# Optimization experiments

Measured on AMD Instinct MI355X. Metric: run time of the kernel, lower is better.

## Reference

```python
import jax, jax.numpy as jnp
import numpy as np

B, T, H, I, O = 64, 1024, 512, 64, 8
NOISE_STD = 0.05
ALPHA = 0.2


def setup_inputs() -> dict:
    key = jax.random.key(0)
    ks = jax.random.split(key, 5)
    return {
        "input": jax.random.normal(ks[0], (B, T, I), dtype=jnp.float32),
        "noise": jax.random.normal(ks[1], (B, T, H), dtype=jnp.float32),
        "wi": jax.random.normal(ks[2], (I, H), dtype=jnp.float32) / np.float32(np.sqrt(H)),
        "si": jnp.ones((I,), jnp.float32),
        # scale so the all-positive effective recurrence |wrec| stays stable over T steps
        "wrec": jax.random.normal(ks[3], (H, H), dtype=jnp.float32) * np.float32(0.5 / H),
        "b": jnp.zeros((H,), jnp.float32),
        "wo": jax.random.normal(ks[4], (H, O), dtype=jnp.float32) / np.float32(H),
        "so": jnp.ones((O,), jnp.float32),
        "wi_mask": jnp.ones((I, H), jnp.float32),
        "wrec_mask": jnp.ones((H, H), jnp.float32),
        "wo_mask": jnp.ones((H, O), jnp.float32),
        "h0": jnp.zeros((H,), jnp.float32),
    }


def reference(input, noise, wi, si, wrec, b, wo, so, wi_mask, wrec_mask, wo_mask, h0):
    batch = input.shape[0]
    # effective weights (constant across timesteps; torch recomputes identical values each step)
    wrec_eff = jnp.abs(wrec) * wrec_mask            # [H, H]
    wi_eff = (wi * si[:, None]) * wi_mask           # [I, H]
    wo_eff = (wo * so[None, :]) * wo_mask           # [H, O]

    h_init = jnp.broadcast_to(h0, (batch, h0.shape[0]))  # [B, H]

    def step(h, xs):
        x_t, n_t = xs                                # [B, I], [B, H]
        r = jax.nn.relu(h)                           # rate from previous state
        h_new = h + NOISE_STD * n_t + ALPHA * (-h + r @ wrec_eff + b + x_t @ wi_eff)
        out_t = jax.nn.relu(h_new) @ wo_eff          # [B, O]
        return h_new, (out_t, h_new)

    xs = (jnp.swapaxes(input, 0, 1), jnp.swapaxes(noise, 0, 1))  # time-major
    _, (outs, hs) = jax.lax.scan(step, h_init, xs)
    output = jnp.swapaxes(outs, 0, 1)                            # [B, T, O]
    trajectories = jnp.concatenate(
        [h_init[:, None, :], jnp.swapaxes(hs, 0, 1)], axis=1     # [B, T+1, H]
    )
    return output, trajectories
```

## Files before the change

### kernel.cpp

```cpp
#include <hip/hip_runtime.h>
#include <hip/hip_bf16.h>
#include <cstddef>
#include <cstdint>

#define BB 64
#define TT 1024
#define HH 512
#define II 64
#define OO 8
#define NOISE_STD 0.05f
#define ALPHA 0.2f

#define G_SLICES 16
#define BT 4
#define NC (BB/BT)
#define K4EXT 160
#define R2STRIDE 328

typedef _Float16 half2_t __attribute__((ext_vector_type(2)));
typedef unsigned int uint32;
typedef uint32 uint4_t __attribute__((ext_vector_type(4)));

#if __has_builtin(__builtin_amdgcn_fdot2)
__device__ __forceinline__ float fdot2f(half2_t a, half2_t b, float c) {
    return __builtin_amdgcn_fdot2(a, b, c, false);
}
#else
__device__ __forceinline__ float fdot2f(half2_t a, half2_t b, float c) {
    return c + (float)a[0] * (float)b[0] + (float)a[1] * (float)b[1];
}
#endif

__device__ __forceinline__ half2_t pkrtz(float a, float b) {
    return __builtin_bit_cast(half2_t, __builtin_amdgcn_cvt_pkrtz(a, b));
}

__device__ __forceinline__ uint4_t load4_sc1(const uint32* p) {
    uint4_t v;
    asm volatile("global_load_dwordx4 %0, %1, off sc1\n\t"
                 "s_waitcnt vmcnt(0)"
                 : "=v"(v) : "v"(p) : "memory");
    return v;
}
__device__ __forceinline__ uint4_t load4_sc0(const uint32* p) {
    uint4_t v;
    asm volatile("global_load_dwordx4 %0, %1, off sc0\n\t"
                 "s_waitcnt vmcnt(0)"
                 : "=v"(v) : "v"(p) : "memory");
    return v;
}
__device__ __forceinline__ void store1_plain(uint32* p, uint32 v) {
    asm volatile("global_store_dword %0, %1, off" :: "v"(p), "v"(v) : "memory");
}

__global__ __launch_bounds__(512, 2)
void rnn_clique(const float* __restrict__ input, const float* __restrict__ noise,
                const float* __restrict__ wi, const float* __restrict__ si,
                const float* __restrict__ wrec, const float* __restrict__ bvec,
                const float* __restrict__ wo, const float* __restrict__ so,
                const float* __restrict__ wi_mask, const float* __restrict__ wrec_mask,
                const float* __restrict__ wo_mask, const float* __restrict__ h0,
                uint32* __restrict__ ex, float* __restrict__ out,
                float* __restrict__ traj)
{
    const int tid  = threadIdx.x;
    const int cq   = blockIdx.x & 15;
    const int sl   = blockIdx.x >> 4;
    const int wv   = tid >> 6;
    const int lane = tid & 63;

    __shared__ half2_t w2[K4EXT * 64];
    __shared__ half2_t r2[2][BT][R2STRIDE];
    __shared__ float   part[BT][8][32];
    __shared__ half2_t wo2[256];
    __shared__ int     mode_sh;

    uint32* aux = ex + (size_t)NC * 2 * BT * HH;

    if (tid == 0) {
        uint32 xcc;
        asm volatile("s_getreg_b32 %0, hwreg(HW_REG_XCC_ID)" : "=s"(xcc));
        xcc &= 0xFFu;
        __hip_atomic_store(aux + cq * 16 + sl, (1u << 16) | xcc,
                           __ATOMIC_RELAXED, __HIP_MEMORY_SCOPE_AGENT);
    }

    {
        const int c = tid & 31, kg = tid >> 5;
        const int gc = sl * 32 + c;
        for (int m = 0; m < 10; ++m) {
            int k4 = m * 16 + kg;
            float v[4];
            #pragma unroll
            for (int q = 0; q < 4; ++q) {
                int kap = k4 * 4 + q;
                float x;
                if (kap < HH) {
                    x = fabsf(wrec[(size_t)kap * HH + gc]) * wrec_mask[(size_t)kap * HH + gc];
                } else if (kap < HH + II) {
                    int i = kap - HH;
                    x = wi[(size_t)i * HH + gc] * si[i] * wi_mask[(size_t)i * HH + gc];
                } else if (kap == HH + II) {
                    x = bvec[gc];
                } else {
                    x = 0.f;
                }
                v[q] = x;
            }
            w2[k4 * 64 + c * 2]     = pkrtz(v[0], v[1]);
            w2[k4 * 64 + c * 2 + 1] = pkrtz(v[2], v[3]);
        }
    }
    if (sl < OO && tid < 256) {
        int k2 = tid, o = sl;
        float v0 = wo[(size_t)(2 * k2) * OO + o] * so[o] * wo_mask[(size_t)(2 * k2) * OO + o];
        float v1 = wo[(size_t)(2 * k2 + 1) * OO + o] * so[o] * wo_mask[(size_t)(2 * k2 + 1) * OO + o];
        wo2[k2] = pkrtz(v0, v1);
    }
    if (tid < 128) {
        int k4 = tid;
        float v0 = fmaxf(h0[4 * k4 + 0], 0.f), v1 = fmaxf(h0[4 * k4 + 1], 0.f);
        float v2 = fmaxf(h0[4 * k4 + 2], 0.f), v3 = fmaxf(h0[4 * k4 + 3], 0.f);
        half2_t p0 = pkrtz(v0, v1), p1 = pkrtz(v2, v3);
        for (int b = 0; b < BT; ++b) { r2[0][b][2 * k4] = p0; r2[0][b][2 * k4 + 1] = p1; }
    }
    if (tid < 8) {
        int par = tid & 1, b = tid >> 1;
        r2[par][b][288] = half2_t{(_Float16)1.f, (_Float16)0.f};
        for (int s = 289; s < R2STRIDE; ++s) r2[par][b][s] = half2_t{(_Float16)0.f, (_Float16)0.f};
    }
    if (wv >= 4 && lane < 32) {
        int b = wv - 4, i2 = lane;
        const float* xp = input + ((size_t)(cq * BT + b) * TT + 0) * II + 2 * i2;
        r2[0][b][256 + i2] = pkrtz(xp[0], xp[1]);
    }

    float h_st = 0.f, n_reg = 0.f, n_reg2 = 0.f;
    float* trajp = nullptr;
    const float* noisep = nullptr;
    uint32* exw = nullptr;
    if (wv < BT && lane < 32) {
        int b = wv, c = lane, gc = sl * 32 + c, bg = cq * BT + b;
        h_st   = h0[gc];
        noisep = noise + (size_t)bg * TT * HH;
        trajp  = traj + (size_t)bg * (TT + 1) * HH;
        n_reg  = noisep[gc];
        n_reg2 = noisep[(size_t)HH + gc];
        trajp[gc] = h_st;
        exw = ex + (size_t)((cq * 2 + 0) * BT + b) * HH + gc;
    }
    __syncthreads();

    const int c_    = lane & 31;
    const int shalf = lane >> 5;
    const int seg   = wv * 2 + shalf;

    half2_t wr[5][4];
    #pragma unroll
    for (int ch = 0; ch < 5; ++ch) {
        int k4b = seg * 10 + ch * 2;
        wr[ch][0] = w2[k4b * 64 + c_ * 2];
        wr[ch][1] = w2[k4b * 64 + c_ * 2 + 1];
        wr[ch][2] = w2[(k4b + 1) * 64 + c_ * 2];
        wr[ch][3] = w2[(k4b + 1) * 64 + c_ * 2 + 1];
    }

    if (wv == 0) {
        uint32 v = (1u << 16);
        for (;;) {
            if (lane < 16)
                v = __hip_atomic_load(aux + cq * 16 + lane,
                                      __ATOMIC_RELAXED, __HIP_MEMORY_SCOPE_AGENT);
            if (__ballot((v >> 16) == 1u) == ~0ull) break;
            __builtin_amdgcn_s_sleep(1);
        }
        uint32 myx = v & 0xFFFFu;
        uint32 x0  = __shfl(myx, 0);
        bool eq = (lane < 16) ? (myx == x0) : true;
        if (lane == 0) mode_sh = (__ballot(eq) == ~0ull) ? 1 : 0;
    }
    __syncthreads();
    const bool local_mode = (mode_sh != 0);

    const int gb  = tid >> 7;
    const int k4g = tid & 127;
    uint32* exg0 = ex + (size_t)((cq * 2 + 0) * BT + gb) * HH + (size_t)(4 * k4g);
    const size_t expar = (size_t)BT * HH;

    for (int t = 0; t < TT; ++t) {
        const int p = t & 1;

        float acc0 = 0.f, acc1 = 0.f, acc2 = 0.f, acc3 = 0.f;
        #pragma unroll
        for (int ch = 0; ch < 5; ++ch) {
            int k2b = seg * 20 + ch * 4;
            {
                half2_t ra = r2[p][0][k2b], rb = r2[p][0][k2b + 1], rc = r2[p][0][k2b + 2], rd = r2[p][0][k2b + 3];
                acc0 = fdot2f(ra, wr[ch][0], acc0); acc0 = fdot2f(rb, wr[ch][1], acc0);
                acc0 = fdot2f(rc, wr[ch][2], acc0); acc0 = fdot2f(rd, wr[ch][3], acc0);
            }
            {
                half2_t ra = r2[p][1][k2b], rb = r2[p][1][k2b + 1], rc = r2[p][1][k2b + 2], rd = r2[p][1][k2b + 3];
                acc1 = fdot2f(ra, wr[ch][0], acc1); acc1 = fdot2f(rb, wr[ch][1], acc1);
                acc1 = fdot2f(rc, wr[ch][2], acc1); acc1 = fdot2f(rd, wr[ch][3], acc1);
            }
            {
                half2_t ra = r2[p][2][k2b], rb = r2[p][2][k2b + 1], rc = r2[p][2][k2b + 2], rd = r2[p][2][k2b + 3];
                acc2 = fdot2f(ra, wr[ch][0], acc2); acc2 = fdot2f(rb, wr[ch][1], acc2);
                acc2 = fdot2f(rc, wr[ch][2], acc2); acc2 = fdot2f(rd, wr[ch][3], acc2);
            }
            {
                half2_t ra = r2[p][3][k2b], rb = r2[p][3][k2b + 1], rc = r2[p][3][k2b + 2], rd = r2[p][3][k2b + 3];
                acc3 = fdot2f(ra, wr[ch][0], acc3); acc3 = fdot2f(rb, wr[ch][1], acc3);
                acc3 = fdot2f(rc, wr[ch][2], acc3); acc3 = fdot2f(rd, wr[ch][3], acc3);
            }
        }
        acc0 += __shfl_xor(acc0, 32);
        acc1 += __shfl_xor(acc1, 32);
        acc2 += __shfl_xor(acc2, 32);
        acc3 += __shfl_xor(acc3, 32);
        if (shalf == 0) {
            part[0][wv][c_] = acc0;
            part[1][wv][c_] = acc1;
            part[2][wv][c_] = acc2;
            part[3][wv][c_] = acc3;
        }
        __syncthreads();

        const uint32 tag = (uint32)(t + 2);
        const size_t poff = (size_t)p * expar;

        if (wv < BT && lane < 32) {
            int b = wv, c = lane, gc = sl * 32 + c;
            float mv = 0.f;
            #pragma unroll
            for (int m = 0; m < 8; ++m) mv += part[b][m][c];
            float hn = (1.f - ALPHA) * h_st + ALPHA * mv + NOISE_STD * n_reg;
            h_st = hn;
            uint32 r16 = __builtin_bit_cast(uint32,
                           __builtin_amdgcn_cvt_pkrtz(fmaxf(hn, 0.f), 0.f)) & 0xFFFFu;
            uint32 word = (tag << 16) | r16;
            if (local_mode) {
                store1_plain(exw + poff, word);
            } else {
                __hip_atomic_store(exw + poff, word,
                                   __ATOMIC_RELAXED, __HIP_MEMORY_SCOPE_AGENT);
            }
            trajp[(size_t)(t + 1) * HH + gc] = hn;
            n_reg = n_reg2;
            int tn = (t + 2 < TT) ? (t + 2) : (TT - 1);
            n_reg2 = noisep[(size_t)tn * HH + gc];
        } else if (wv >= 4) {
            if (sl < OO && t > 0) {
                int b = wv - 4;
                int k2 = lane * 4;
                float q = 0.f;
                q = fdot2f(r2[p][b][k2],     wo2[k2],     q);
                q = fdot2f(r2[p][b][k2 + 1], wo2[k2 + 1], q);
                q = fdot2f(r2[p][b][k2 + 2], wo2[k2 + 2], q);
                q = fdot2f(r2[p][b][k2 + 3], wo2[k2 + 3], q);
                #pragma unroll
                for (int d = 32; d >= 1; d >>= 1) q += __shfl_xor(q, d);
                if (lane == 0) out[((size_t)(cq * BT + b) * TT + (t - 1)) * OO + sl] = q;
            }
            if (lane < 32) {
                int b = wv - 4, i2 = lane;
                int tn = (t + 1 < TT) ? (t + 1) : (TT - 1);
                const float* xp = input + ((size_t)(cq * BT + b) * TT + tn) * II + 2 * i2;
                r2[p ^ 1][b][256 + i2] = pkrtz(xp[0], xp[1]);
            }
        }

        {
            const uint32* g0 = exg0 + poff;
            uint4_t w;
            int spins = 0;
            if (local_mode) {
                for (;;) {
                    w = load4_sc0(g0);
                    if ((w[0] >> 16) == tag && (w[1] >> 16) == tag &&
                        (w[2] >> 16) == tag && (w[3] >> 16) == tag) break;
                    if (++spins > 8) __builtin_amdgcn_s_sleep(1);
                }
            } else {
                for (;;) {
                    w = load4_sc1(g0);
                    if ((w[0] >> 16) == tag && (w[1] >> 16) == tag &&
                        (w[2] >> 16) == tag && (w[3] >> 16) == tag) break;
                    __builtin_amdgcn_s_sleep(1);
                }
            }
            uint32 q0 = (w[0] & 0xFFFFu) | (w[1] << 16);
            uint32 q1 = (w[2] & 0xFFFFu) | (w[3] << 16);
            r2[p ^ 1][gb][2 * k4g]     = __builtin_bit_cast(half2_t, q0);
            r2[p ^ 1][gb][2 * k4g + 1] = __builtin_bit_cast(half2_t, q1);
        }
        __syncthreads();
    }

    if (wv >= 4 && sl < OO) {
        int b = wv - 4;
        int k2 = lane * 4;
        float q = 0.f;
        q = fdot2f(r2[0][b][k2],     wo2[k2],     q);
        q = fdot2f(r2[0][b][k2 + 1], wo2[k2 + 1], q);
        q = fdot2f(r2[0][b][k2 + 2], wo2[k2 + 2], q);
        q = fdot2f(r2[0][b][k2 + 3], wo2[k2 + 3], q);
        #pragma unroll
        for (int d = 32; d >= 1; d >>= 1) q += __shfl_xor(q, d);
        if (lane == 0) out[((size_t)(cq * BT + b) * TT + (TT - 1)) * OO + sl] = q;
    }
}

extern "C" void kernel_launch(void* const* d_in, const int* in_sizes, int n_in,
                              void* d_out, int out_size, void* d_ws, size_t ws_size,
                              hipStream_t stream) {
    const float* input     = (const float*)d_in[0];
    const float* noise     = (const float*)d_in[1];
    const float* wi        = (const float*)d_in[2];
    const float* si        = (const float*)d_in[3];
    const float* wrec      = (const float*)d_in[4];
    const float* bvec      = (const float*)d_in[5];
    const float* wo        = (const float*)d_in[6];
    const float* so        = (const float*)d_in[7];
    const float* wi_mask   = (const float*)d_in[8];
    const float* wrec_mask = (const float*)d_in[9];
    const float* wo_mask   = (const float*)d_in[10];
    const float* h0        = (const float*)d_in[11];

    float* out  = (float*)d_out;
    float* traj = out + (size_t)BB * TT * OO;
    uint32* ex  = (uint32*)d_ws;

    (void)hipMemsetAsync(d_ws, 0,
        (size_t)(NC * 2 * BT * HH + NC * G_SLICES) * sizeof(uint32), stream);

    rnn_clique<<<dim3(NC * G_SLICES), dim3(512), 0, stream>>>(
        input, noise, wi, si, wrec, bvec, wo, so,
        wi_mask, wrec_mask, wo_mask, h0, ex, out, traj);
}
```

Before: 1.608 ms.

## Interleave two batch groups per block to hide cross-block exchange latency

Each block now handles two groups of four batch rows (A and B) instead of one, which halves the grid to 128 blocks. The time loop alternates between the two groups: the matvec for one group runs while the other group's exchanged hidden state is still in flight through global memory. The aim is to hide the spin-wait latency of the cross-block sync behind useful compute. In exchange each block does twice the work per step with extra __syncthreads, fewer CUs are used, and more LDS is needed for the doubled r2 buffers. The local-mode spin threshold also goes from 8 to 16.

Measured after the change: 3.017 ms. 87.6% more time.

```diff
diff --git a/kernel.cpp b/kernel.cpp
--- a/kernel.cpp
+++ b/kernel.cpp
@@ -11,11 +11,14 @@
 #define NOISE_STD 0.05f
 #define ALPHA 0.2f
 
-#define G_SLICES 16
+#define NCL 8
+#define SLICES 16
 #define BT 4
-#define NC (BB/BT)
 #define K4EXT 160
 #define R2STRIDE 328
+
+#define EXGRP (2 * BT * HH)
+#define EXCQ  (2 * EXGRP)
 
 typedef _Float16 half2_t __attribute__((ext_vector_type(2)));
 typedef unsigned int uint32;
@@ -64,24 +67,24 @@
                 float* __restrict__ traj)
 {
     const int tid  = threadIdx.x;
-    const int cq   = blockIdx.x & 15;
-    const int sl   = blockIdx.x >> 4;
+    const int cq   = blockIdx.x & 7;
+    const int sl   = blockIdx.x >> 3;
     const int wv   = tid >> 6;
     const int lane = tid & 63;
 
     __shared__ half2_t w2[K4EXT * 64];
-    __shared__ half2_t r2[2][BT][R2STRIDE];
+    __shared__ half2_t r2[2][2][BT][R2STRIDE];
     __shared__ float   part[BT][8][32];
     __shared__ half2_t wo2[256];
     __shared__ int     mode_sh;
 
-    uint32* aux = ex + (size_t)NC * 2 * BT * HH;
+    uint32* aux = ex + (size_t)NCL * EXCQ;
 
     if (tid == 0) {
         uint32 xcc;
         asm volatile("s_getreg_b32 %0, hwreg(HW_REG_XCC_ID)" : "=s"(xcc));
         xcc &= 0xFFu;
-        __hip_atomic_store(aux + cq * 16 + sl, (1u << 16) | xcc,
+        __hip_atomic_store(aux + cq * SLICES + sl, (1u << 16) | xcc,
                            __ATOMIC_RELAXED, __HIP_MEMORY_SCOPE_AGENT);
     }
 
@@ -122,32 +125,41 @@
         float v0 = fmaxf(h0[4 * k4 + 0], 0.f), v1 = fmaxf(h0[4 * k4 + 1], 0.f);
         float v2 = fmaxf(h0[4 * k4 + 2], 0.f), v3 = fmaxf(h0[4 * k4 + 3], 0.f);
         half2_t p0 = pkrtz(v0, v1), p1 = pkrtz(v2, v3);
-        for (int b = 0; b < BT; ++b) { r2[0][b][2 * k4] = p0; r2[0][b][2 * k4 + 1] = p1; }
-    }
-    if (tid < 8) {
-        int par = tid & 1, b = tid >> 1;
-        r2[par][b][288] = half2_t{(_Float16)1.f, (_Float16)0.f};
-        for (int s = 289; s < R2STRIDE; ++s) r2[par][b][s] = half2_t{(_Float16)0.f, (_Float16)0.f};
+        for (int g = 0; g < 2; ++g)
+            for (int b = 0; b < BT; ++b) {
+                r2[g][0][b][2 * k4] = p0; r2[g][0][b][2 * k4 + 1] = p1;
+            }
+    }
+    if (tid < 16) {
+        int g = tid & 1, par = (tid >> 1) & 1, b = tid >> 2;
+        r2[g][par][b][288] = half2_t{(_Float16)1.f, (_Float16)0.f};
+        for (int s = 289; s < R2STRIDE; ++s) r2[g][par][b][s] = half2_t{(_Float16)0.f, (_Float16)0.f};
     }
     if (wv >= 4 && lane < 32) {
         int b = wv - 4, i2 = lane;
-        const float* xp = input + ((size_t)(cq * BT + b) * TT + 0) * II + 2 * i2;
-        r2[0][b][256 + i2] = pkrtz(xp[0], xp[1]);
-    }
-
-    float h_st = 0.f, n_reg = 0.f, n_reg2 = 0.f;
-    float* trajp = nullptr;
-    const float* noisep = nullptr;
-    uint32* exw = nullptr;
+        const float* xpA = input + ((size_t)(cq * 8 + b) * TT + 0) * II + 2 * i2;
+        const float* xpB = input + ((size_t)(cq * 8 + 4 + b) * TT + 0) * II + 2 * i2;
+        r2[0][0][b][256 + i2] = pkrtz(xpA[0], xpA[1]);
+        r2[1][0][b][256 + i2] = pkrtz(xpB[0], xpB[1]);
+    }
+
+    float hA = 0.f, hB = 0.f, nA0 = 0.f, nA1 = 0.f, nB0 = 0.f, nB1 = 0.f;
+    float *trajpA = nullptr, *trajpB = nullptr;
+    const float *noisepA = nullptr, *noisepB = nullptr;
+    uint32 *exwA = nullptr, *exwB = nullptr;
     if (wv < BT && lane < 32) {
-        int b = wv, c = lane, gc = sl * 32 + c, bg = cq * BT + b;
-        h_st   = h0[gc];
-        noisep = noise + (size_t)bg * TT * HH;
-        trajp  = traj + (size_t)bg * (TT + 1) * HH;
-        n_reg  = noisep[gc];
-        n_reg2 = noisep[(size_t)HH + gc];
-        trajp[gc] = h_st;
-        exw = ex + (size_t)((cq * 2 + 0) * BT + b) * HH + gc;
+        int b = wv, c = lane, gc = sl * 32 + c;
+        int bgA = cq * 8 + b, bgB = cq * 8 + 4 + b;
+        hA = h0[gc]; hB = hA;
+        noisepA = noise + (size_t)bgA * TT * HH;
+        noisepB = noise + (size_t)bgB * TT * HH;
+        trajpA  = traj + (size_t)bgA * (TT + 1) * HH;
+        trajpB  = traj + (size_t)bgB * (TT + 1) * HH;
+        nA0 = noisepA[gc];              nB0 = noisepB[gc];
+        nA1 = noisepA[(size_t)HH + gc]; nB1 = noisepB[(size_t)HH + gc];
+        trajpA[gc] = hA; trajpB[gc] = hB;
+        exwA = ex + (size_t)cq * EXCQ + (size_t)b * HH + gc;
+        exwB = exwA + EXGRP;
     }
     __syncthreads();
 
@@ -168,15 +180,15 @@
     if (wv == 0) {
         uint32 v = (1u << 16);
         for (;;) {
-            if (lane < 16)
-                v = __hip_atomic_load(aux + cq * 16 + lane,
+            if (lane < SLICES)
+                v = __hip_atomic_load(aux + cq * SLICES + lane,
                                       __ATOMIC_RELAXED, __HIP_MEMORY_SCOPE_AGENT);
             if (__ballot((v >> 16) == 1u) == ~0ull) break;
             __builtin_amdgcn_s_sleep(1);
         }
         uint32 myx = v & 0xFFFFu;
         uint32 x0  = __shfl(myx, 0);
-        bool eq = (lane < 16) ? (myx == x0) : true;
+        bool eq = (lane < SLICES) ? (myx == x0) : true;
         if (lane == 0) mode_sh = (__ballot(eq) == ~0ull) ? 1 : 0;
     }
     __syncthreads();
@@ -184,131 +196,187 @@
 
     const int gb  = tid >> 7;
     const int k4g = tid & 127;
-    uint32* exg0 = ex + (size_t)((cq * 2 + 0) * BT + gb) * HH + (size_t)(4 * k4g);
-    const size_t expar = (size_t)BT * HH;
+    uint32* exgA = ex + (size_t)cq * EXCQ + (size_t)gb * HH + (size_t)(4 * k4g);
+    uint32* exgB = exgA + EXGRP;
+
+#define MATVEC(G, P)                                                              \
+    {                                                                             \
+        float a0 = 0.f, a1 = 0.f, a2 = 0.f, a3 = 0.f;                             \
+        _Pragma("unroll")                                                         \
+        for (int ch = 0; ch < 5; ++ch) {                                          \
+            int k2b = seg * 20 + ch * 4;                                          \
+            {                                                                     \
+                half2_t ra = r2[G][P][0][k2b],     rb = r2[G][P][0][k2b + 1];     \
+                half2_t rc = r2[G][P][0][k2b + 2], rd = r2[G][P][0][k2b + 3];     \
+                a0 = fdot2f(ra, wr[ch][0], a0); a0 = fdot2f(rb, wr[ch][1], a0);   \
+                a0 = fdot2f(rc, wr[ch][2], a0); a0 = fdot2f(rd, wr[ch][3], a0);   \
+            }                                                                     \
+            {                                                                     \
+                half2_t ra = r2[G][P][1][k2b],     rb = r2[G][P][1][k2b + 1];     \
+                half2_t rc = r2[G][P][1][k2b + 2], rd = r2[G][P][1][k2b + 3];     \
+                a1 = fdot2f(ra, wr[ch][0], a1); a1 = fdot2f(rb, wr[ch][1], a1);   \
+                a1 = fdot2f(rc, wr[ch][2], a1); a1 = fdot2f(rd, wr[ch][3], a1);   \
+            }                                                                     \
+            {                                                                     \
+                half2_t ra = r2[G][P][2][k2b],     rb = r2[G][P][2][k2b + 1];     \
+                half2_t rc = r2[G][P][2][k2b + 2], rd = r2[G][P][2][k2b + 3];     \
+                a2 = fdot2f(ra, wr[ch][0], a2); a2 = fdot2f(rb, wr[ch][1], a2);   \
+                a2 = fdot2f(rc, wr[ch][2], a2); a2 = fdot2f(rd, wr[ch][3], a2);   \
+            }                                                                     \
+            {                                                                     \
+                half2_t ra = r2[G][P][3][k2b],     rb = r2[G][P][3][k2b + 1];     \
+                half2_t rc = r2[G][P][3][k2b + 2], rd = r2[G][P][3][k2b + 3];     \
+                a3 = fdot2f(ra, wr[ch][0], a3); a3 = fdot2f(rb, wr[ch][1], a3);   \
+                a3 = fdot2f(rc, wr[ch][2], a3); a3 = fdot2f(rd, wr[ch][3], a3);   \
+            }                                                                     \
+        }                                                                         \
+        a0 += __shfl_xor(a0, 32); a1 += __shfl_xor(a1, 32);                       \
+        a2 += __shfl_xor(a2, 32); a3 += __shfl_xor(a3, 32);                       \
+        if (shalf == 0) {                                                         \
+            part[0][wv][c_] = a0; part[1][wv][c_] = a1;                           \
+            part[2][wv][c_] = a2; part[3][wv][c_] = a3;                           \
+        }                                                                         \
+    }
+
+#define GATHER(EXG, PAR, TAG, G, P2)                                              \
+    {                                                                             \
+        const uint32* g0 = (EXG) + (size_t)(PAR) * (BT * HH);                     \
+        uint4_t w; int spins = 0;                                                 \
+        if (local_mode) {                                                         \
+            for (;;) {                                                            \
+                w = load4_sc0(g0);                                                \
+                if ((w[0] >> 16) == (TAG) && (w[1] >> 16) == (TAG) &&             \
+                    (w[2] >> 16) == (TAG) && (w[3] >> 16) == (TAG)) break;        \
+                if (++spins > 16) __builtin_amdgcn_s_sleep(1);                    \
+            }                                                                     \
+        } else {                                                                  \
+            for (;;) {                                                            \
+                w = load4_sc1(g0);                                                \
+                if ((w[0] >> 16) == (TAG) && (w[1] >> 16) == (TAG) &&             \
+                    (w[2] >> 16) == (TAG) && (w[3] >> 16) == (TAG)) break;        \
+                __builtin_amdgcn_s_sleep(1);                                      \
+            }                                                                     \
+        }                                                                         \
+        uint32 q0 = (w[0] & 0xFFFFu) | (w[1] << 16);                              \
+        uint32 q1 = (w[2] & 0xFFFFu) | (w[3] << 16);                              \
+        r2[G][P2][gb][2 * k4g]     = __builtin_bit_cast(half2_t, q0);             \
+        r2[G][P2][gb][2 * k4g + 1] = __builtin_bit_cast(half2_t, q1);             \
+    }
 
     for (int t = 0; t < TT; ++t) {
         const int p = t & 1;
-
-        float acc0 = 0.f, acc1 = 0.f, acc2 = 0.f, acc3 = 0.f;
-        #pragma unroll
-        for (int ch = 0; ch < 5; ++ch) {
-            int k2b = seg * 20 + ch * 4;
-            {
-                half2_t ra = r2[p][0][k2b], rb = r2[p][0][k2b + 1], rc = r2[p][0][k2b + 2], rd = r2[p][0][k2b + 3];
-                acc0 = fdot2f(ra, wr[ch][0], acc0); acc0 = fdot2f(rb, wr[ch][1], acc0);
-                acc0 = fdot2f(rc, wr[ch][2], acc0); acc0 = fdot2f(rd, wr[ch][3], acc0);
-            }
-            {
-                half2_t ra = r2[p][1][k2b], rb = r2[p][1][k2b + 1], rc = r2[p][1][k2b + 2], rd = r2[p][1][k2b + 3];
-                acc1 = fdot2f(ra, wr[ch][0], acc1); acc1 = fdot2f(rb, wr[ch][1], acc1);
-                acc1 = fdot2f(rc, wr[ch][2], acc1); acc1 = fdot2f(rd, wr[ch][3], acc1);
-            }
-            {
-                half2_t ra = r2[p][2][k2b], rb = r2[p][2][k2b + 1], rc = r2[p][2][k2b + 2], rd = r2[p][2][k2b + 3];
-                acc2 = fdot2f(ra, wr[ch][0], acc2); acc2 = fdot2f(rb, wr[ch][1], acc2);
-                acc2 = fdot2f(rc, wr[ch][2], acc2); acc2 = fdot2f(rd, wr[ch][3], acc2);
-            }
-            {
-                half2_t ra = r2[p][3][k2b], rb = r2[p][3][k2b + 1], rc = r2[p][3][k2b + 2], rd = r2[p][3][k2b + 3];
-                acc3 = fdot2f(ra, wr[ch][0], acc3); acc3 = fdot2f(rb, wr[ch][1], acc3);
-                acc3 = fdot2f(rc, wr[ch][2], acc3); acc3 = fdot2f(rd, wr[ch][3], acc3);
-            }
-        }
-        acc0 += __shfl_xor(acc0, 32);
-        acc1 += __shfl_xor(acc1, 32);
-        acc2 += __shfl_xor(acc2, 32);
-        acc3 += __shfl_xor(acc3, 32);
-        if (shalf == 0) {
-            part[0][wv][c_] = acc0;
-            part[1][wv][c_] = acc1;
-            part[2][wv][c_] = acc2;
-            part[3][wv][c_] = acc3;
-        }
+        const uint32 tagN = (uint32)(t + 2);
+
+        MATVEC(0, p);
         __syncthreads();
-
-        const uint32 tag = (uint32)(t + 2);
-        const size_t poff = (size_t)p * expar;
 
         if (wv < BT && lane < 32) {
             int b = wv, c = lane, gc = sl * 32 + c;
             float mv = 0.f;
             #pragma unroll
             for (int m = 0; m < 8; ++m) mv += part[b][m][c];
-            float hn = (1.f - ALPHA) * h_st + ALPHA * mv + NOISE_STD * n_reg;
-            h_st = hn;
+            float hn = (1.f - ALPHA) * hA + ALPHA * mv + NOISE_STD * nA0;
+            hA = hn;
             uint32 r16 = __builtin_bit_cast(uint32,
                            __builtin_amdgcn_cvt_pkrtz(fmaxf(hn, 0.f), 0.f)) & 0xFFFFu;
-            uint32 word = (tag << 16) | r16;
-            if (local_mode) {
-                store1_plain(exw + poff, word);
-            } else {
-                __hip_atomic_store(exw + poff, word,
-                                   __ATOMIC_RELAXED, __HIP_MEMORY_SCOPE_AGENT);
-            }
-            trajp[(size_t)(t + 1) * HH + gc] = hn;
-            n_reg = n_reg2;
+            uint32 word = (tagN << 16) | r16;
+            if (local_mode) store1_plain(exwA + (size_t)(p ^ 1) * (BT * HH), word);
+            else __hip_atomic_store(exwA + (size_t)(p ^ 1) * (BT * HH), word,
+                                    __ATOMIC_RELAXED, __HIP_MEMORY_SCOPE_AGENT);
+            trajpA[(size_t)(t + 1) * HH + gc] = hn;
+            nA0 = nA1;
+        }
+        if (t > 0) GATHER(exgB, p, (uint32)(t + 1), 1, p);
+        if (wv < BT && lane < 32) {
+            int gc = sl * 32 + lane;
             int tn = (t + 2 < TT) ? (t + 2) : (TT - 1);
-            n_reg2 = noisep[(size_t)tn * HH + gc];
+            nA1 = noisepA[(size_t)tn * HH + gc];
         } else if (wv >= 4) {
             if (sl < OO && t > 0) {
-                int b = wv - 4;
-                int k2 = lane * 4;
+                int b = wv - 4, k2 = lane * 4;
                 float q = 0.f;
-                q = fdot2f(r2[p][b][k2],     wo2[k2],     q);
-                q = fdot2f(r2[p][b][k2 + 1], wo2[k2 + 1], q);
-                q = fdot2f(r2[p][b][k2 + 2], wo2[k2 + 2], q);
-                q = fdot2f(r2[p][b][k2 + 3], wo2[k2 + 3], q);
+                q = fdot2f(r2[0][p][b][k2],     wo2[k2],     q);
+                q = fdot2f(r2[0][p][b][k2 + 1], wo2[k2 + 1], q);
+                q = fdot2f(r2[0][p][b][k2 + 2], wo2[k2 + 2], q);
+                q = fdot2f(r2[0][p][b][k2 + 3], wo2[k2 + 3], q);
                 #pragma unroll
                 for (int d = 32; d >= 1; d >>= 1) q += __shfl_xor(q, d);
-                if (lane == 0) out[((size_t)(cq * BT + b) * TT + (t - 1)) * OO + sl] = q;
+                if (lane == 0) out[((size_t)(cq * 8 + b) * TT + (t - 1)) * OO + sl] = q;
             }
             if (lane < 32) {
                 int b = wv - 4, i2 = lane;
                 int tn = (t + 1 < TT) ? (t + 1) : (TT - 1);
-                const float* xp = input + ((size_t)(cq * BT + b) * TT + tn) * II + 2 * i2;
-                r2[p ^ 1][b][256 + i2] = pkrtz(xp[0], xp[1]);
-            }
-        }
-
-        {
-            const uint32* g0 = exg0 + poff;
-            uint4_t w;
-            int spins = 0;
-            if (local_mode) {
-                for (;;) {
-                    w = load4_sc0(g0);
-                    if ((w[0] >> 16) == tag && (w[1] >> 16) == tag &&
-                        (w[2] >> 16) == tag && (w[3] >> 16) == tag) break;
-                    if (++spins > 8) __builtin_amdgcn_s_sleep(1);
-                }
-            } else {
-                for (;;) {
-                    w = load4_sc1(g0);
-                    if ((w[0] >> 16) == tag && (w[1] >> 16) == tag &&
-                        (w[2] >> 16) == tag && (w[3] >> 16) == tag) break;
-                    __builtin_amdgcn_s_sleep(1);
-                }
-            }
-            uint32 q0 = (w[0] & 0xFFFFu) | (w[1] << 16);
-            uint32 q1 = (w[2] & 0xFFFFu) | (w[3] << 16);
-            r2[p ^ 1][gb][2 * k4g]     = __builtin_bit_cast(half2_t, q0);
-            r2[p ^ 1][gb][2 * k4g + 1] = __builtin_bit_cast(half2_t, q1);
+                const float* xp = input + ((size_t)(cq * 8 + b) * TT + tn) * II + 2 * i2;
+                r2[0][p ^ 1][b][256 + i2] = pkrtz(xp[0], xp[1]);
+            }
         }
         __syncthreads();
-    }
-
+
+        MATVEC(1, p);
+        __syncthreads();
+
+        if (wv < BT && lane < 32) {
+            int b = wv, c = lane, gc = sl * 32 + c;
+            float mv = 0.f;
+            #pragma unroll
+            for (int m = 0; m < 8; ++m) mv += part[b][m][c];
+            float hn = (1.f - ALPHA) * hB + ALPHA * mv + NOISE_STD * nB0;
+            hB = hn;
+            uint32 r16 = __builtin_bit_cast(uint32,
+                           __builtin_amdgcn_cvt_pkrtz(fmaxf(hn, 0.f), 0.f)) & 0xFFFFu;
+            uint32 word = (tagN << 16) | r16;
+            if (local_mode) store1_plain(exwB + (size_t)(p ^ 1) * (BT * HH), word);
+            else __hip_atomic_store(exwB + (size_t)(p ^ 1) * (BT * HH), word,
+                                    __ATOMIC_RELAXED, __HIP_MEMORY_SCOPE_AGENT);
+            trajpB[(size_t)(t + 1) * HH + gc] = hn;
+            nB0 = nB1;
+        }
+        GATHER(exgA, p ^ 1, tagN, 0, p ^ 1);
+        if (wv < BT && lane < 32) {
+            int gc = sl * 32 + lane;
+            int tn = (t + 2 < TT) ? (t + 2) : (TT - 1);
+            nB1 = noisepB[(size_t)tn * HH + gc];
+        } else if (wv >= 4) {
+            if (sl < OO && t > 0) {
+                int b = wv - 4, k2 = lane * 4;
+                float q = 0.f;
+                q = fdot2f(r2[1][p][b][k2],     wo2[k2],     q);
+                q = fdot2f(r2[1][p][b][k2 + 1], wo2[k2 + 1], q);
+                q = fdot2f(r2[1][p][b][k2 + 2], wo2[k2 + 2], q);
+                q = fdot2f(r2[1][p][b][k2 + 3], wo2[k2 + 3], q);
+                #pragma unroll
+                for (int d = 32; d >= 1; d >>= 1) q += __shfl_xor(q, d);
+                if (lane == 0) out[((size_t)(cq * 8 + 4 + b) * TT + (t - 1)) * OO + sl] = q;
+            }
+            if (lane < 32) {
+                int b = wv - 4, i2 = lane;
+                int tn = (t + 1 < TT) ? (t + 1) : (TT - 1);
+                const float* xp = input + ((size_t)(cq * 8 + 4 + b) * TT + tn) * II + 2 * i2;
+                r2[1][p ^ 1][b][256 + i2] = pkrtz(xp[0], xp[1]);
+            }
+        }
+        __syncthreads();
+    }
+
+    GATHER(exgB, 0, (uint32)(TT + 1), 1, 0);
+    __syncthreads();
     if (wv >= 4 && sl < OO) {
-        int b = wv - 4;
-        int k2 = lane * 4;
-        float q = 0.f;
-        q = fdot2f(r2[0][b][k2],     wo2[k2],     q);
-        q = fdot2f(r2[0][b][k2 + 1], wo2[k2 + 1], q);
-        q = fdot2f(r2[0][b][k2 + 2], wo2[k2 + 2], q);
-        q = fdot2f(r2[0][b][k2 + 3], wo2[k2 + 3], q);
+        int b = wv - 4, k2 = lane * 4;
+        float qa = 0.f, qb = 0.f;
+        qa = fdot2f(r2[0][0][b][k2],     wo2[k2],     qa);
+        qa = fdot2f(r2[0][0][b][k2 + 1], wo2[k2 + 1], qa);
+        qa = fdot2f(r2[0][0][b][k2 + 2], wo2[k2 + 2], qa);
+        qa = fdot2f(r2[0][0][b][k2 + 3], wo2[k2 + 3], qa);
+        qb = fdot2f(r2[1][0][b][k2],     wo2[k2],     qb);
+        qb = fdot2f(r2[1][0][b][k2 + 1], wo2[k2 + 1], qb);
+        qb = fdot2f(r2[1][0][b][k2 + 2], wo2[k2 + 2], qb);
+        qb = fdot2f(r2[1][0][b][k2 + 3], wo2[k2 + 3], qb);
         #pragma unroll
-        for (int d = 32; d >= 1; d >>= 1) q += __shfl_xor(q, d);
-        if (lane == 0) out[((size_t)(cq * BT + b) * TT + (TT - 1)) * OO + sl] = q;
+        for (int d = 32; d >= 1; d >>= 1) { qa += __shfl_xor(qa, d); qb += __shfl_xor(qb, d); }
+        if (lane == 0) {
+            out[((size_t)(cq * 8 + b) * TT + (TT - 1)) * OO + sl] = qa;
+            out[((size_t)(cq * 8 + 4 + b) * TT + (TT - 1)) * OO + sl] = qb;
+        }
     }
 }
 
@@ -333,9 +401,9 @@
     uint32* ex  = (uint32*)d_ws;
 
     (void)hipMemsetAsync(d_ws, 0,
-        (size_t)(NC * 2 * BT * HH + NC * G_SLICES) * sizeof(uint32), stream);
-
-    rnn_clique<<<dim3(NC * G_SLICES), dim3(512), 0, stream>>>(
+        (size_t)(NCL * EXCQ + NCL * SLICES) * sizeof(uint32), stream);
+
+    rnn_clique<<<dim3(NCL * SLICES), dim3(512), 0, stream>>>(
         input, noise, wi, si, wrec, bvec, wo, so,
         wi_mask, wrec_mask, wo_mask, h0, ex, out, traj);
 }
```

## Repartition recurrence into per-batch 4-block cliques with register-resident weights

Applied to the files above, without the earlier changes.

The work is re-split from 16 cliques, each handling 4 batch rows across 16 column slices, to 64 cliques, each handling one batch row across 4 blocks of 128 columns. Each thread now keeps its 80 packed weight pairs in registers, which removes the shared-memory weight staging and the wave-level shuffle reduction. The cross-block exchange per step involves only 4 producer blocks, which should cut synchronisation latency on the serial time loop. The trade-offs are higher register pressure and only 128 threads doing the exchange and state update each step. The local-mode spin threshold before sleeping is also raised.

Result: slower. 1.784 ms (+10.9%).

```diff
diff --git a/kernel.cpp b/kernel.cpp
--- a/kernel.cpp
+++ b/kernel.cpp
@@ -11,11 +11,9 @@
 #define NOISE_STD 0.05f
 #define ALPHA 0.2f
 
-#define G_SLICES 16
-#define BT 4
-#define NC (BB/BT)
-#define K4EXT 160
-#define R2STRIDE 328
+#define NCLQ 64
+#define SLC 4
+#define EXCQ (2 * HH)
 
 typedef _Float16 half2_t __attribute__((ext_vector_type(2)));
 typedef unsigned int uint32;
@@ -54,187 +52,134 @@
 }
 
 __global__ __launch_bounds__(512, 2)
-void rnn_clique(const float* __restrict__ input, const float* __restrict__ noise,
-                const float* __restrict__ wi, const float* __restrict__ si,
-                const float* __restrict__ wrec, const float* __restrict__ bvec,
-                const float* __restrict__ wo, const float* __restrict__ so,
-                const float* __restrict__ wi_mask, const float* __restrict__ wrec_mask,
-                const float* __restrict__ wo_mask, const float* __restrict__ h0,
-                uint32* __restrict__ ex, float* __restrict__ out,
-                float* __restrict__ traj)
+void rnn_b1(const float* __restrict__ input, const float* __restrict__ noise,
+            const float* __restrict__ wi, const float* __restrict__ si,
+            const float* __restrict__ wrec, const float* __restrict__ bvec,
+            const float* __restrict__ wo, const float* __restrict__ so,
+            const float* __restrict__ wi_mask, const float* __restrict__ wrec_mask,
+            const float* __restrict__ wo_mask, const float* __restrict__ h0,
+            uint32* __restrict__ ex, float* __restrict__ out,
+            float* __restrict__ traj)
 {
     const int tid  = threadIdx.x;
-    const int cq   = blockIdx.x & 15;
-    const int sl   = blockIdx.x >> 4;
+    const int cq   = blockIdx.x & 63;
+    const int sl   = blockIdx.x >> 6;
     const int wv   = tid >> 6;
     const int lane = tid & 63;
-
-    __shared__ half2_t w2[K4EXT * 64];
-    __shared__ half2_t r2[2][BT][R2STRIDE];
-    __shared__ float   part[BT][8][32];
-    __shared__ half2_t wo2[256];
+    const int c    = tid & 127;
+    const int ks   = tid >> 7;
+    const int gc   = sl * 128 + c;
+
+    __shared__ half2_t r2[2][336];
+    __shared__ float   part[4][128];
+    __shared__ half2_t wo2[2][256];
     __shared__ int     mode_sh;
 
-    uint32* aux = ex + (size_t)NC * 2 * BT * HH;
+    uint32* aux = ex + (size_t)NCLQ * EXCQ;
 
     if (tid == 0) {
         uint32 xcc;
         asm volatile("s_getreg_b32 %0, hwreg(HW_REG_XCC_ID)" : "=s"(xcc));
-        xcc &= 0xFFu;
-        __hip_atomic_store(aux + cq * 16 + sl, (1u << 16) | xcc,
+        __hip_atomic_store(aux + cq * SLC + sl, (1u << 16) | (xcc & 0xFFu),
                            __ATOMIC_RELAXED, __HIP_MEMORY_SCOPE_AGENT);
     }
 
+    half2_t wr[80];
+    #pragma unroll
+    for (int j = 0; j < 80; ++j) {
+        int k0 = (ks * 80 + j) * 2;
+        int k1 = k0 + 1;
+        float v0, v1;
+        if (k0 < HH)           v0 = fabsf(wrec[(size_t)k0 * HH + gc]) * wrec_mask[(size_t)k0 * HH + gc];
+        else if (k0 < HH + II) { int i = k0 - HH; v0 = wi[(size_t)i * HH + gc] * si[i] * wi_mask[(size_t)i * HH + gc]; }
+        else if (k0 == HH + II)  v0 = bvec[gc];
+        else                     v0 = 0.f;
+        if (k1 < HH)           v1 = fabsf(wrec[(size_t)k1 * HH + gc]) * wrec_mask[(size_t)k1 * HH + gc];
+        else if (k1 < HH + II) { int i = k1 - HH; v1 = wi[(size_t)i * HH + gc] * si[i] * wi_mask[(size_t)i * HH + gc]; }
+        else if (k1 == HH + II)  v1 = bvec[gc];
+        else                     v1 = 0.f;
+        wr[j] = pkrtz(v0, v1);
+    }
+
     {
-        const int c = tid & 31, kg = tid >> 5;
-        const int gc = sl * 32 + c;
-        for (int m = 0; m < 10; ++m) {
-            int k4 = m * 16 + kg;
-            float v[4];
-            #pragma unroll
-            for (int q = 0; q < 4; ++q) {
-                int kap = k4 * 4 + q;
-                float x;
-                if (kap < HH) {
-                    x = fabsf(wrec[(size_t)kap * HH + gc]) * wrec_mask[(size_t)kap * HH + gc];
-                } else if (kap < HH + II) {
-                    int i = kap - HH;
-                    x = wi[(size_t)i * HH + gc] * si[i] * wi_mask[(size_t)i * HH + gc];
-                } else if (kap == HH + II) {
-                    x = bvec[gc];
-                } else {
-                    x = 0.f;
-                }
-                v[q] = x;
-            }
-            w2[k4 * 64 + c * 2]     = pkrtz(v[0], v[1]);
-            w2[k4 * 64 + c * 2 + 1] = pkrtz(v[2], v[3]);
-        }
-    }
-    if (sl < OO && tid < 256) {
-        int k2 = tid, o = sl;
-        float v0 = wo[(size_t)(2 * k2) * OO + o] * so[o] * wo_mask[(size_t)(2 * k2) * OO + o];
+        int oo = tid >> 8, k2 = tid & 255, o = sl * 2 + oo;
+        float v0 = wo[(size_t)(2 * k2) * OO + o]     * so[o] * wo_mask[(size_t)(2 * k2) * OO + o];
         float v1 = wo[(size_t)(2 * k2 + 1) * OO + o] * so[o] * wo_mask[(size_t)(2 * k2 + 1) * OO + o];
-        wo2[k2] = pkrtz(v0, v1);
-    }
+        wo2[oo][k2] = pkrtz(v0, v1);
+    }
+    if (tid < 256) {
+        float v0 = fmaxf(h0[2 * tid], 0.f), v1 = fmaxf(h0[2 * tid + 1], 0.f);
+        r2[0][tid] = pkrtz(v0, v1);
+    }
+    if (tid >= 256 && tid < 352) {
+        int r = tid - 256;
+        int par = r & 1, s = 288 + (r >> 1);
+        r2[par][s] = (s == 288) ? half2_t{(_Float16)1.f, (_Float16)0.f}
+                                : half2_t{(_Float16)0.f, (_Float16)0.f};
+    }
+    if (wv == 6 && lane < 32) {
+        const float* xp = input + ((size_t)cq * TT + 0) * II + 2 * lane;
+        r2[0][256 + lane] = pkrtz(xp[0], xp[1]);
+    }
+
+    float h_st = 0.f, n_reg = 0.f, n_nxt = 0.f;
+    const float* noisep = nullptr;
+    float* trajp = nullptr;
+    uint32* exw = nullptr;
+    int gcf = 0;
     if (tid < 128) {
-        int k4 = tid;
-        float v0 = fmaxf(h0[4 * k4 + 0], 0.f), v1 = fmaxf(h0[4 * k4 + 1], 0.f);
-        float v2 = fmaxf(h0[4 * k4 + 2], 0.f), v3 = fmaxf(h0[4 * k4 + 3], 0.f);
-        half2_t p0 = pkrtz(v0, v1), p1 = pkrtz(v2, v3);
-        for (int b = 0; b < BT; ++b) { r2[0][b][2 * k4] = p0; r2[0][b][2 * k4 + 1] = p1; }
-    }
-    if (tid < 8) {
-        int par = tid & 1, b = tid >> 1;
-        r2[par][b][288] = half2_t{(_Float16)1.f, (_Float16)0.f};
-        for (int s = 289; s < R2STRIDE; ++s) r2[par][b][s] = half2_t{(_Float16)0.f, (_Float16)0.f};
-    }
-    if (wv >= 4 && lane < 32) {
-        int b = wv - 4, i2 = lane;
-        const float* xp = input + ((size_t)(cq * BT + b) * TT + 0) * II + 2 * i2;
-        r2[0][b][256 + i2] = pkrtz(xp[0], xp[1]);
-    }
-
-    float h_st = 0.f, n_reg = 0.f, n_reg2 = 0.f;
-    float* trajp = nullptr;
-    const float* noisep = nullptr;
-    uint32* exw = nullptr;
-    if (wv < BT && lane < 32) {
-        int b = wv, c = lane, gc = sl * 32 + c, bg = cq * BT + b;
-        h_st   = h0[gc];
-        noisep = noise + (size_t)bg * TT * HH;
-        trajp  = traj + (size_t)bg * (TT + 1) * HH;
-        n_reg  = noisep[gc];
-        n_reg2 = noisep[(size_t)HH + gc];
-        trajp[gc] = h_st;
-        exw = ex + (size_t)((cq * 2 + 0) * BT + b) * HH + gc;
+        gcf    = sl * 128 + tid;
+        noisep = noise + (size_t)cq * TT * HH;
+        trajp  = traj + (size_t)cq * (TT + 1) * HH;
+        h_st   = h0[gcf];
+        n_reg  = noisep[gcf];
+        n_nxt  = noisep[(size_t)HH + gcf];
+        trajp[gcf] = h_st;
+        exw = ex + (size_t)cq * EXCQ + gcf;
     }
     __syncthreads();
-
-    const int c_    = lane & 31;
-    const int shalf = lane >> 5;
-    const int seg   = wv * 2 + shalf;
-
-    half2_t wr[5][4];
-    #pragma unroll
-    for (int ch = 0; ch < 5; ++ch) {
-        int k4b = seg * 10 + ch * 2;
-        wr[ch][0] = w2[k4b * 64 + c_ * 2];
-        wr[ch][1] = w2[k4b * 64 + c_ * 2 + 1];
-        wr[ch][2] = w2[(k4b + 1) * 64 + c_ * 2];
-        wr[ch][3] = w2[(k4b + 1) * 64 + c_ * 2 + 1];
-    }
 
     if (wv == 0) {
         uint32 v = (1u << 16);
         for (;;) {
-            if (lane < 16)
-                v = __hip_atomic_load(aux + cq * 16 + lane,
+            if (lane < SLC)
+                v = __hip_atomic_load(aux + cq * SLC + lane,
                                       __ATOMIC_RELAXED, __HIP_MEMORY_SCOPE_AGENT);
             if (__ballot((v >> 16) == 1u) == ~0ull) break;
             __builtin_amdgcn_s_sleep(1);
         }
         uint32 myx = v & 0xFFFFu;
         uint32 x0  = __shfl(myx, 0);
-        bool eq = (lane < 16) ? (myx == x0) : true;
+        bool eq = (lane < SLC) ? (myx == x0) : true;
         if (lane == 0) mode_sh = (__ballot(eq) == ~0ull) ? 1 : 0;
     }
     __syncthreads();
     const bool local_mode = (mode_sh != 0);
 
-    const int gb  = tid >> 7;
-    const int k4g = tid & 127;
-    uint32* exg0 = ex + (size_t)((cq * 2 + 0) * BT + gb) * HH + (size_t)(4 * k4g);
-    const size_t expar = (size_t)BT * HH;
+    uint32* exg0 = ex + (size_t)cq * EXCQ + 4 * (tid & 127);
 
     for (int t = 0; t < TT; ++t) {
         const int p = t & 1;
 
-        float acc0 = 0.f, acc1 = 0.f, acc2 = 0.f, acc3 = 0.f;
+        float acc = 0.f;
         #pragma unroll
-        for (int ch = 0; ch < 5; ++ch) {
-            int k2b = seg * 20 + ch * 4;
-            {
-                half2_t ra = r2[p][0][k2b], rb = r2[p][0][k2b + 1], rc = r2[p][0][k2b + 2], rd = r2[p][0][k2b + 3];
-                acc0 = fdot2f(ra, wr[ch][0], acc0); acc0 = fdot2f(rb, wr[ch][1], acc0);
-                acc0 = fdot2f(rc, wr[ch][2], acc0); acc0 = fdot2f(rd, wr[ch][3], acc0);
-            }
-            {
-                half2_t ra = r2[p][1][k2b], rb = r2[p][1][k2b + 1], rc = r2[p][1][k2b + 2], rd = r2[p][1][k2b + 3];
-                acc1 = fdot2f(ra, wr[ch][0], acc1); acc1 = fdot2f(rb, wr[ch][1], acc1);
-                acc1 = fdot2f(rc, wr[ch][2], acc1); acc1 = fdot2f(rd, wr[ch][3], acc1);
-            }
-            {
-                half2_t ra = r2[p][2][k2b], rb = r2[p][2][k2b + 1], rc = r2[p][2][k2b + 2], rd = r2[p][2][k2b + 3];
-                acc2 = fdot2f(ra, wr[ch][0], acc2); acc2 = fdot2f(rb, wr[ch][1], acc2);
-                acc2 = fdot2f(rc, wr[ch][2], acc2); acc2 = fdot2f(rd, wr[ch][3], acc2);
-            }
-            {
-                half2_t ra = r2[p][3][k2b], rb = r2[p][3][k2b + 1], rc = r2[p][3][k2b + 2], rd = r2[p][3][k2b + 3];
-                acc3 = fdot2f(ra, wr[ch][0], acc3); acc3 = fdot2f(rb, wr[ch][1], acc3);
-                acc3 = fdot2f(rc, wr[ch][2], acc3); acc3 = fdot2f(rd, wr[ch][3], acc3);
-            }
+        for (int ch = 0; ch < 20; ++ch) {
+            int s = ks * 80 + ch * 4;
+            half2_t ra = r2[p][s],     rb = r2[p][s + 1];
+            half2_t rc = r2[p][s + 2], rd = r2[p][s + 3];
+            acc = fdot2f(ra, wr[4 * ch],     acc);
+            acc = fdot2f(rb, wr[4 * ch + 1], acc);
+            acc = fdot2f(rc, wr[4 * ch + 2], acc);
+            acc = fdot2f(rd, wr[4 * ch + 3], acc);
         }
-        acc0 += __shfl_xor(acc0, 32);
-        acc1 += __shfl_xor(acc1, 32);
-        acc2 += __shfl_xor(acc2, 32);
-        acc3 += __shfl_xor(acc3, 32);
-        if (shalf == 0) {
-            part[0][wv][c_] = acc0;
-            part[1][wv][c_] = acc1;
-            part[2][wv][c_] = acc2;
-            part[3][wv][c_] = acc3;
-        }
+        part[ks][c] = acc;
         __syncthreads();
 
-        const uint32 tag = (uint32)(t + 2);
-        const size_t poff = (size_t)p * expar;
-
-        if (wv < BT && lane < 32) {
-            int b = wv, c = lane, gc = sl * 32 + c;
-            float mv = 0.f;
-            #pragma unroll
-            for (int m = 0; m < 8; ++m) mv += part[b][m][c];
+        const uint32 tag  = (uint32)(t + 2);
+        const int    poff = p * HH;
+
+        if (tid < 128) {
+            float mv = part[0][tid] + part[1][tid] + part[2][tid] + part[3][tid];
             float hn = (1.f - ALPHA) * h_st + ALPHA * mv + NOISE_STD * n_reg;
             h_st = hn;
             uint32 r16 = __builtin_bit_cast(uint32,
@@ -246,32 +191,7 @@
                 __hip_atomic_store(exw + poff, word,
                                    __ATOMIC_RELAXED, __HIP_MEMORY_SCOPE_AGENT);
             }
-            trajp[(size_t)(t + 1) * HH + gc] = hn;
-            n_reg = n_reg2;
-            int tn = (t + 2 < TT) ? (t + 2) : (TT - 1);
-            n_reg2 = noisep[(size_t)tn * HH + gc];
-        } else if (wv >= 4) {
-            if (sl < OO && t > 0) {
-                int b = wv - 4;
-                int k2 = lane * 4;
-                float q = 0.f;
-                q = fdot2f(r2[p][b][k2],     wo2[k2],     q);
-                q = fdot2f(r2[p][b][k2 + 1], wo2[k2 + 1], q);
-                q = fdot2f(r2[p][b][k2 + 2], wo2[k2 + 2], q);
-                q = fdot2f(r2[p][b][k2 + 3], wo2[k2 + 3], q);
-                #pragma unroll
-                for (int d = 32; d >= 1; d >>= 1) q += __shfl_xor(q, d);
-                if (lane == 0) out[((size_t)(cq * BT + b) * TT + (t - 1)) * OO + sl] = q;
-            }
-            if (lane < 32) {
-                int b = wv - 4, i2 = lane;
-                int tn = (t + 1 < TT) ? (t + 1) : (TT - 1);
-                const float* xp = input + ((size_t)(cq * BT + b) * TT + tn) * II + 2 * i2;
-                r2[p ^ 1][b][256 + i2] = pkrtz(xp[0], xp[1]);
-            }
-        }
-
-        {
+
             const uint32* g0 = exg0 + poff;
             uint4_t w;
             int spins = 0;
@@ -280,7 +200,7 @@
                     w = load4_sc0(g0);
                     if ((w[0] >> 16) == tag && (w[1] >> 16) == tag &&
                         (w[2] >> 16) == tag && (w[3] >> 16) == tag) break;
-                    if (++spins > 8) __builtin_amdgcn_s_sleep(1);
+                    if (++spins > 16) __builtin_amdgcn_s_sleep(1);
                 }
             } else {
                 for (;;) {
@@ -292,23 +212,45 @@
             }
             uint32 q0 = (w[0] & 0xFFFFu) | (w[1] << 16);
             uint32 q1 = (w[2] & 0xFFFFu) | (w[3] << 16);
-            r2[p ^ 1][gb][2 * k4g]     = __builtin_bit_cast(half2_t, q0);
-            r2[p ^ 1][gb][2 * k4g + 1] = __builtin_bit_cast(half2_t, q1);
+            r2[p ^ 1][2 * tid]     = __builtin_bit_cast(half2_t, q0);
+            r2[p ^ 1][2 * tid + 1] = __builtin_bit_cast(half2_t, q1);
+
+            trajp[(size_t)(t + 1) * HH + gcf] = h_st;
+            n_reg = n_nxt;
+            int tn = (t + 2 < TT) ? (t + 2) : (TT - 1);
+            n_nxt = noisep[(size_t)tn * HH + gcf];
+        } else if (wv == 4 || wv == 5) {
+            if (t > 0) {
+                int oo = wv - 4, o = sl * 2 + oo;
+                int k2 = lane * 4;
+                float q = 0.f;
+                q = fdot2f(r2[p][k2],     wo2[oo][k2],     q);
+                q = fdot2f(r2[p][k2 + 1], wo2[oo][k2 + 1], q);
+                q = fdot2f(r2[p][k2 + 2], wo2[oo][k2 + 2], q);
+                q = fdot2f(r2[p][k2 + 3], wo2[oo][k2 + 3], q);
+                #pragma unroll
+                for (int d = 32; d >= 1; d >>= 1) q += __shfl_xor(q, d);
+                if (lane == 0) out[((size_t)cq * TT + (t - 1)) * OO + o] = q;
+            }
+        } else if (wv == 6 && lane < 32) {
+            int tn = (t + 1 < TT) ? (t + 1) : (TT - 1);
+            const float* xp = input + ((size_t)cq * TT + tn) * II + 2 * lane;
+            r2[p ^ 1][256 + lane] = pkrtz(xp[0], xp[1]);
         }
         __syncthreads();
     }
 
-    if (wv >= 4 && sl < OO) {
-        int b = wv - 4;
+    if (wv == 4 || wv == 5) {
+        int oo = wv - 4, o = sl * 2 + oo;
         int k2 = lane * 4;
         float q = 0.f;
-        q = fdot2f(r2[0][b][k2],     wo2[k2],     q);
-        q = fdot2f(r2[0][b][k2 + 1], wo2[k2 + 1], q);
-        q = fdot2f(r2[0][b][k2 + 2], wo2[k2 + 2], q);
-        q = fdot2f(r2[0][b][k2 + 3], wo2[k2 + 3], q);
+        q = fdot2f(r2[0][k2],     wo2[oo][k2],     q);
+        q = fdot2f(r2[0][k2 + 1], wo2[oo][k2 + 1], q);
+        q = fdot2f(r2[0][k2 + 2], wo2[oo][k2 + 2], q);
+        q = fdot2f(r2[0][k2 + 3], wo2[oo][k2 + 3], q);
         #pragma unroll
         for (int d = 32; d >= 1; d >>= 1) q += __shfl_xor(q, d);
-        if (lane == 0) out[((size_t)(cq * BT + b) * TT + (TT - 1)) * OO + sl] = q;
+        if (lane == 0) out[((size_t)cq * TT + (TT - 1)) * OO + o] = q;
     }
 }
 
@@ -333,9 +275,9 @@
     uint32* ex  = (uint32*)d_ws;
 
     (void)hipMemsetAsync(d_ws, 0,
-        (size_t)(NC * 2 * BT * HH + NC * G_SLICES) * sizeof(uint32), stream);
-
-    rnn_clique<<<dim3(NC * G_SLICES), dim3(512), 0, stream>>>(
+        (size_t)(NCLQ * EXCQ + NCLQ * SLC) * sizeof(uint32), stream);
+
+    rnn_b1<<<dim3(NCLQ * SLC), dim3(512), 0, stream>>>(
         input, noise, wi, si, wrec, bvec, wo, so,
         wi_mask, wrec_mask, wo_mask, h0, ex, out, traj);
 }
```
